# Kernel optimization log

Measured on AMD Instinct MI355X. Metric: run time of the kernel, lower is better.

The kernel has to match this reference:

```python
import jax, jax.numpy as jnp
import numpy as np

NUM_HIDDEN = 128
NUM_IN = 256
NUM_HEADS = 4
B, T, N, K = 4, 32, 96, 30


def setup_inputs() -> dict:
    key = jax.random.key(0)
    ks = jax.random.split(key, 7)
    return {
        "h_V": jax.random.normal(ks[0], (B, T, N, NUM_HIDDEN), dtype=jnp.float32),
        "h_EV": jax.random.normal(ks[1], (B, T, N, K, NUM_IN), dtype=jnp.float32),
        "mask_attend": jax.random.randint(ks[2], (B, T, N, K), 0, 2, dtype=jnp.int32),
        "Wq": jax.random.normal(ks[3], (NUM_HIDDEN, NUM_HIDDEN), dtype=jnp.float32) / np.sqrt(NUM_HIDDEN),
        "Wk": jax.random.normal(ks[4], (NUM_IN, NUM_HIDDEN), dtype=jnp.float32) / np.sqrt(NUM_IN),
        "Wv": jax.random.normal(ks[5], (NUM_IN, NUM_HIDDEN), dtype=jnp.float32) / np.sqrt(NUM_IN),
        "Wo": jax.random.normal(ks[6], (NUM_HIDDEN, NUM_HIDDEN), dtype=jnp.float32) / np.sqrt(NUM_HIDDEN),
    }


def reference(h_V, h_EV, mask_attend, Wq, Wk, Wv, Wo):
    b, t, n, k = h_EV.shape[:4]
    h = NUM_HEADS
    d = NUM_HIDDEN // h
    # projections
    Q = (h_V @ Wq).reshape(b, t, n, h, d)            # [B,T,N,H,d]
    Kp = (h_EV @ Wk).reshape(b, t, n, k, h, d)       # [B,T,N,K,H,d]
    V = (h_EV @ Wv).reshape(b, t, n, k, h, d)        # [B,T,N,K,H,d]
    # per-node neighbor attention logits [B,T,N,H,K]
    logits = jnp.einsum('btnhd,btnkhd->btnhk', Q, Kp) / jnp.sqrt(jnp.float32(d))
    neg_inf = jnp.finfo(jnp.float32).min
    mask = mask_attend[:, :, :, None, :]             # [B,T,N,1,K] -> broadcast over heads
    logits = jnp.where(mask > 0, logits, neg_inf)
    attend = jax.nn.softmax(logits, axis=-1)
    attend = attend * mask.astype(jnp.float32)
    # combine values: [B,T,N,H,d]
    out = jnp.einsum('btnhk,btnkhd->btnhd', attend, V).reshape(b, t, n, NUM_HIDDEN)
    return out @ Wo
```

## Files before the change

### kernel.cpp

```cpp
#include <hip/hip_runtime.h>
#include <hip/hip_bf16.h>
#include <cfloat>
#include <math.h>

constexpr int SITES = 12288;
constexpr int KNB   = 30;
constexpr int CIN   = 256;
#define RSQRT_D 0.17677669529663689f

typedef short bf16x8 __attribute__((ext_vector_type(8)));
typedef float f32x4  __attribute__((ext_vector_type(4)));

__device__ inline unsigned short f2bs(float x) {
    __hip_bfloat16 b = __float2bfloat16(x);
    return *(unsigned short*)&b;
}
__device__ inline float bs2f(unsigned short u) {
    unsigned int v = (unsigned int)u << 16;
    float f;
    __builtin_memcpy(&f, &v, 4);
    return f;
}
__device__ inline unsigned int pack2(float a, float b) {
    return (unsigned int)f2bs(a) | ((unsigned int)f2bs(b) << 16);
}

__global__ __launch_bounds__(256) void precompute_w(
    const float* __restrict__ Wq, const float* __restrict__ Wk,
    const float* __restrict__ Wv, const float* __restrict__ Wo,
    unsigned short* __restrict__ Mt, unsigned short* __restrict__ W3t) {
    int gid = blockIdx.x * 256 + threadIdx.x;
    if (gid < 131072) {
        int p = gid >> 7;
        int i = gid & 127;
        int h = p >> 8;
        int c = p & 255;
        const float4* wq = (const float4*)(Wq + (size_t)i * 128 + h * 32);
        const float4* wk = (const float4*)(Wk + (size_t)c * 128 + h * 32);
        float s = 0.f;
        #pragma unroll
        for (int d = 0; d < 8; ++d) {
            float4 a = wq[d], b = wk[d];
            s += a.x * b.x; s += a.y * b.y; s += a.z * b.z; s += a.w * b.w;
        }
        Mt[gid] = f2bs(s);
    } else {
        int o = gid - 131072;
        int p = o >> 7;
        int j = o & 127;
        int h = p >> 8;
        int c = p & 255;
        const float* wv = Wv + (size_t)c * 128 + h * 32;
        const float* wo = Wo + (size_t)(h * 32) * 128 + j;
        float s = 0.f;
        #pragma unroll
        for (int d = 0; d < 32; ++d)
            s += wv[d] * wo[(size_t)d * 128];
        W3t[(size_t)j * 1024 + p] = f2bs(s);
    }
}

template <bool OUT_BF16, bool A_F32>
__global__ __launch_bounds__(256) void gemm_bt_bf16(
    const void* __restrict__ Aptr, const unsigned short* __restrict__ Bt,
    void* __restrict__ C, int M, int N, int K) {
    constexpr int BM = 64, BN = 128, BK = 32, PAD = 8;
    constexpr int NT = BN / 16;
    __shared__ unsigned short As[BM][BK + PAD];
    __shared__ unsigned short Bs[BN][BK + PAD];
    const int tid  = threadIdx.x;
    const int wave = tid >> 6;
    const int lane = tid & 63;
    const int quad = lane >> 4;
    const int l16  = lane & 15;
    const int bm0 = blockIdx.x * BM;
    const int bn0 = blockIdx.y * BN;

    f32x4 acc[NT];
    #pragma unroll
    for (int j = 0; j < NT; ++j) acc[j] = (f32x4){0.f, 0.f, 0.f, 0.f};

    for (int kk = 0; kk < K; kk += BK) {
        {
            int row = tid >> 2, off = (tid & 3) * 8;
            if (A_F32) {
                const float* Af = (const float*)Aptr;
                const float4* src = (const float4*)&Af[(size_t)(bm0 + row) * K + kk + off];
                float4 a0 = src[0], a1 = src[1];
                uint4 p;
                p.x = pack2(a0.x, a0.y); p.y = pack2(a0.z, a0.w);
                p.z = pack2(a1.x, a1.y); p.w = pack2(a1.z, a1.w);
                *(uint4*)&As[row][off] = p;
            } else {
                const unsigned short* Ab = (const unsigned short*)Aptr;
                *(uint4*)&As[row][off] =
                    *(const uint4*)&Ab[(size_t)(bm0 + row) * K + kk + off];
            }
        }
        #pragma unroll
        for (int i = 0; i < 2; ++i) {
            int c2 = tid * 2 + i;
            int brow = c2 >> 2, boff = (c2 & 3) * 8;
            *(uint4*)&Bs[brow][boff] =
                *(const uint4*)&Bt[(size_t)(bn0 + brow) * K + kk + boff];
        }
        __syncthreads();
        bf16x8 af = *(const bf16x8*)&As[wave * 16 + l16][quad * 8];
        #pragma unroll
        for (int j = 0; j < NT; ++j) {
            bf16x8 bf = *(const bf16x8*)&Bs[j * 16 + l16][quad * 8];
            acc[j] = __builtin_amdgcn_mfma_f32_16x16x32_bf16(af, bf, acc[j], 0, 0, 0);
        }
        __syncthreads();
    }
    int row0 = bm0 + wave * 16 + quad * 4;
    #pragma unroll
    for (int j = 0; j < NT; ++j) {
        int col = bn0 + j * 16 + l16;
        #pragma unroll
        for (int r = 0; r < 4; ++r) {
            if (OUT_BF16)
                ((unsigned short*)C)[(size_t)(row0 + r) * N + col] = f2bs(acc[j][r]);
            else
                ((float*)C)[(size_t)(row0 + r) * N + col] = acc[j][r];
        }
    }
}

__global__ __launch_bounds__(256) void attn_kernel(
    const float* __restrict__ hEV, const int* __restrict__ mask,
    const unsigned short* __restrict__ qt, unsigned short* __restrict__ evb) {
    __shared__ unsigned short evS[KNB * CIN];
    __shared__ float qS[1024];
    __shared__ float logitsL[4 * 32];
    __shared__ float attendL[4 * 32];
    __shared__ int   activeS[32];
    __shared__ int   naS;

    const int s = blockIdx.x;
    const int tid = threadIdx.x;
    const int lane = tid & 63;
    const int wv = tid >> 6;
    const int hw = lane >> 5;
    const int sl = lane & 31;

    if (tid < 64) {
        int mk = (tid < KNB) ? mask[(size_t)s * KNB + tid] : 0;
        unsigned long long bal = __ballot(mk > 0);
        if (tid == 0) naS = __popcll(bal);
        if (mk > 0) activeS[__popcll(bal & ((1ull << tid) - 1))] = tid;
    } else if (tid < 192) {
        int t2 = tid - 64;
        uint4 u = ((const uint4*)(qt + (size_t)s * 1024))[t2];
        float f[8];
        f[0] = bs2f(u.x & 0xffff); f[1] = bs2f(u.x >> 16);
        f[2] = bs2f(u.y & 0xffff); f[3] = bs2f(u.y >> 16);
        f[4] = bs2f(u.z & 0xffff); f[5] = bs2f(u.z >> 16);
        f[6] = bs2f(u.w & 0xffff); f[7] = bs2f(u.w >> 16);
        *(float4*)&qS[t2 * 8]     = *(float4*)&f[0];
        *(float4*)&qS[t2 * 8 + 4] = *(float4*)&f[4];
    }
    __syncthreads();

    float qf[4][8];
    #pragma unroll
    for (int h = 0; h < 4; ++h) {
        *(float4*)&qf[h][0] = *(const float4*)&qS[h * 256 + sl * 8];
        *(float4*)&qf[h][4] = *(const float4*)&qS[h * 256 + sl * 8 + 4];
    }
    const int na = naS;

    for (int r = wv * 2 + hw; r < na; r += 8) {
        int k = activeS[r];
        const float* row = hEV + (size_t)s * (KNB * CIN) + (size_t)k * CIN + sl * 8;
        float4 v0 = *(const float4*)row;
        float4 v1 = *(const float4*)(row + 4);

        uint4 p;
        p.x = pack2(v0.x, v0.y); p.y = pack2(v0.z, v0.w);
        p.z = pack2(v1.x, v1.y); p.w = pack2(v1.z, v1.w);
        *(uint4*)&evS[r * CIN + sl * 8] = p;

        float l[4];
        #pragma unroll
        for (int h = 0; h < 4; ++h) {
            l[h] = v0.x * qf[h][0] + v0.y * qf[h][1] + v0.z * qf[h][2] + v0.w * qf[h][3]
                 + v1.x * qf[h][4] + v1.y * qf[h][5] + v1.z * qf[h][6] + v1.w * qf[h][7];
        }
        #pragma unroll
        for (int m = 1; m < 32; m <<= 1) {
            #pragma unroll
            for (int h = 0; h < 4; ++h) l[h] += __shfl_xor(l[h], m, 64);
        }
        if (sl == 0) {
            #pragma unroll
            for (int h = 0; h < 4; ++h) logitsL[h * 32 + r] = l[h] * RSQRT_D;
        }
    }
    __syncthreads();

    {
        float lg = (lane < na) ? logitsL[wv * 32 + lane] : -FLT_MAX;
        float mx = lg;
        #pragma unroll
        for (int m = 1; m < 64; m <<= 1) mx = fmaxf(mx, __shfl_xor(mx, m, 64));
        float e = (lane < na) ? __expf(lg - mx) : 0.f;
        float sm = e;
        #pragma unroll
        for (int m = 1; m < 64; m <<= 1) sm += __shfl_xor(sm, m, 64);
        if (lane < na) attendL[wv * 32 + lane] = e / sm;
    }
    __syncthreads();

    float a0 = 0.f, a1 = 0.f, a2 = 0.f, a3 = 0.f;
    for (int r = 0; r < na; ++r) {
        float evv = bs2f(evS[r * CIN + tid]);
        a0 = fmaf(attendL[r], evv, a0);
        a1 = fmaf(attendL[32 + r], evv, a1);
        a2 = fmaf(attendL[64 + r], evv, a2);
        a3 = fmaf(attendL[96 + r], evv, a3);
    }
    size_t ob = (size_t)s * 1024 + tid;
    evb[ob]       = f2bs(a0);
    evb[ob + 256] = f2bs(a1);
    evb[ob + 512] = f2bs(a2);
    evb[ob + 768] = f2bs(a3);
}

extern "C" void kernel_launch(void* const* d_in, const int* in_sizes, int n_in,
                              void* d_out, int out_size, void* d_ws, size_t ws_size,
                              hipStream_t stream) {
    const float* hV   = (const float*)d_in[0];
    const float* hEV  = (const float*)d_in[1];
    const int*   mask = (const int*)d_in[2];
    const float* Wq   = (const float*)d_in[3];
    const float* Wk   = (const float*)d_in[4];
    const float* Wv   = (const float*)d_in[5];
    const float* Wo   = (const float*)d_in[6];
    float* out = (float*)d_out;

    unsigned short* ws = (unsigned short*)d_ws;
    unsigned short* Mt   = ws;
    unsigned short* W3t  = ws + 131072;
    unsigned short* qt   = ws + 262144;
    unsigned short* evb  = qt + (size_t)SITES * 1024;
    size_t need = ((size_t)262144 + 2 * (size_t)SITES * 1024) * 2;
    if (ws_size < need) return;

    precompute_w<<<dim3(1024), dim3(256), 0, stream>>>(Wq, Wk, Wv, Wo, Mt, W3t);

    gemm_bt_bf16<true, true><<<dim3(SITES / 64, 1024 / 128), dim3(256), 0, stream>>>(
        hV, Mt, qt, SITES, 1024, 128);

    attn_kernel<<<dim3(SITES), dim3(256), 0, stream>>>(hEV, mask, qt, evb);

    gemm_bt_bf16<false, false><<<dim3(SITES / 64, 1), dim3(256), 0, stream>>>(
        evb, W3t, out, SITES, 128, 1024);
}
```

Baseline: 511.9 us.

## Prefetch GEMM tiles, split-K final GEMM with atomics, batch attention row loads

The GEMM kernel now prefetches the next K-slice of A and B into registers while the current tile is consumed. The final projection GEMM is split along K into four chunks that accumulate into the output with atomic adds. The output is zeroed by extra blocks added to the weight-precompute kernel. The Q GEMM uses a wider BN=256 tile, and the attention kernel issues all of a thread's neighbour-row loads up front before computing logits. The aim is more memory-level parallelism and better occupancy for the final GEMM, which had only 192 blocks. In exchange it adds atomic traffic, nondeterministic summation order, and more registers per thread.

Measured after the change: 531.9 us. +3.9%, slower.

```diff
diff --git a/kernel.cpp b/kernel.cpp
--- a/kernel.cpp
+++ b/kernel.cpp
@@ -28,7 +28,16 @@
 __global__ __launch_bounds__(256) void precompute_w(
     const float* __restrict__ Wq, const float* __restrict__ Wk,
     const float* __restrict__ Wv, const float* __restrict__ Wo,
-    unsigned short* __restrict__ Mt, unsigned short* __restrict__ W3t) {
+    unsigned short* __restrict__ Mt, unsigned short* __restrict__ W3t,
+    float* __restrict__ outZ) {
+    if (blockIdx.x >= 1024) {
+        int idx = (blockIdx.x - 1024) * 256 + threadIdx.x;
+        float4 z = {0.f, 0.f, 0.f, 0.f};
+        float4* o4 = (float4*)outZ;
+        #pragma unroll
+        for (int j = 0; j < 4; ++j) o4[(size_t)j * 98304 + idx] = z;
+        return;
+    }
     int gid = blockIdx.x * 256 + threadIdx.x;
     if (gid < 131072) {
         int p = gid >> 7;
@@ -60,12 +69,13 @@
     }
 }
 
-template <bool OUT_BF16, bool A_F32>
+template <int BN, bool OUT_BF16, bool A_F32, bool ATOMIC>
 __global__ __launch_bounds__(256) void gemm_bt_bf16(
     const void* __restrict__ Aptr, const unsigned short* __restrict__ Bt,
-    void* __restrict__ C, int M, int N, int K) {
-    constexpr int BM = 64, BN = 128, BK = 32, PAD = 8;
-    constexpr int NT = BN / 16;
+    void* __restrict__ C, int M, int N, int K, int Kc) {
+    constexpr int BM = 64, BK = 32, PAD = 8;
+    constexpr int NT  = BN / 16;
+    constexpr int BCH = (BN * BK) / (8 * 256);
     __shared__ unsigned short As[BM][BK + PAD];
     __shared__ unsigned short Bs[BN][BK + PAD];
     const int tid  = threadIdx.x;
@@ -75,41 +85,64 @@
     const int l16  = lane & 15;
     const int bm0 = blockIdx.x * BM;
     const int bn0 = blockIdx.y * BN;
+    const int k0  = blockIdx.z * Kc;
+    const int arow = tid >> 2, aoff = (tid & 3) * 8;
 
     f32x4 acc[NT];
     #pragma unroll
     for (int j = 0; j < NT; ++j) acc[j] = (f32x4){0.f, 0.f, 0.f, 0.f};
 
-    for (int kk = 0; kk < K; kk += BK) {
-        {
-            int row = tid >> 2, off = (tid & 3) * 8;
+    const float* Af = (const float*)Aptr;
+    const unsigned short* Ab = (const unsigned short*)Aptr;
+
+    float4 af0, af1; uint4 apre; uint4 bpre[BCH];
+    {
+        if (A_F32) {
+            const float4* src = (const float4*)&Af[(size_t)(bm0 + arow) * K + k0 + aoff];
+            af0 = src[0]; af1 = src[1];
+        } else {
+            apre = *(const uint4*)&Ab[(size_t)(bm0 + arow) * K + k0 + aoff];
+        }
+        #pragma unroll
+        for (int i = 0; i < BCH; ++i) {
+            int c2 = i * 256 + tid;
+            bpre[i] = *(const uint4*)&Bt[(size_t)(bn0 + (c2 >> 2)) * K + k0 + (c2 & 3) * 8];
+        }
+    }
+    for (int kk = k0; kk < k0 + Kc; kk += BK) {
+        if (A_F32) {
+            uint4 p;
+            p.x = pack2(af0.x, af0.y); p.y = pack2(af0.z, af0.w);
+            p.z = pack2(af1.x, af1.y); p.w = pack2(af1.z, af1.w);
+            *(uint4*)&As[arow][aoff] = p;
+        } else {
+            *(uint4*)&As[arow][aoff] = apre;
+        }
+        #pragma unroll
+        for (int i = 0; i < BCH; ++i) {
+            int c2 = i * 256 + tid;
+            *(uint4*)&Bs[c2 >> 2][(c2 & 3) * 8] = bpre[i];
+        }
+        __syncthreads();
+        int kn = kk + BK;
+        if (kn < k0 + Kc) {
             if (A_F32) {
-                const float* Af = (const float*)Aptr;
-                const float4* src = (const float4*)&Af[(size_t)(bm0 + row) * K + kk + off];
-                float4 a0 = src[0], a1 = src[1];
-                uint4 p;
-                p.x = pack2(a0.x, a0.y); p.y = pack2(a0.z, a0.w);
-                p.z = pack2(a1.x, a1.y); p.w = pack2(a1.z, a1.w);
-                *(uint4*)&As[row][off] = p;
+                const float4* src = (const float4*)&Af[(size_t)(bm0 + arow) * K + kn + aoff];
+                af0 = src[0]; af1 = src[1];
             } else {
-                const unsigned short* Ab = (const unsigned short*)Aptr;
-                *(uint4*)&As[row][off] =
-                    *(const uint4*)&Ab[(size_t)(bm0 + row) * K + kk + off];
-            }
-        }
-        #pragma unroll
-        for (int i = 0; i < 2; ++i) {
-            int c2 = tid * 2 + i;
-            int brow = c2 >> 2, boff = (c2 & 3) * 8;
-            *(uint4*)&Bs[brow][boff] =
-                *(const uint4*)&Bt[(size_t)(bn0 + brow) * K + kk + boff];
-        }
-        __syncthreads();
-        bf16x8 af = *(const bf16x8*)&As[wave * 16 + l16][quad * 8];
+                apre = *(const uint4*)&Ab[(size_t)(bm0 + arow) * K + kn + aoff];
+            }
+            #pragma unroll
+            for (int i = 0; i < BCH; ++i) {
+                int c2 = i * 256 + tid;
+                bpre[i] = *(const uint4*)&Bt[(size_t)(bn0 + (c2 >> 2)) * K + kn + (c2 & 3) * 8];
+            }
+        }
+        bf16x8 afr = *(const bf16x8*)&As[wave * 16 + l16][quad * 8];
         #pragma unroll
         for (int j = 0; j < NT; ++j) {
-            bf16x8 bf = *(const bf16x8*)&Bs[j * 16 + l16][quad * 8];
-            acc[j] = __builtin_amdgcn_mfma_f32_16x16x32_bf16(af, bf, acc[j], 0, 0, 0);
+            bf16x8 bfr = *(const bf16x8*)&Bs[j * 16 + l16][quad * 8];
+            acc[j] = __builtin_amdgcn_mfma_f32_16x16x32_bf16(afr, bfr, acc[j], 0, 0, 0);
         }
         __syncthreads();
     }
@@ -119,10 +152,13 @@
         int col = bn0 + j * 16 + l16;
         #pragma unroll
         for (int r = 0; r < 4; ++r) {
-            if (OUT_BF16)
-                ((unsigned short*)C)[(size_t)(row0 + r) * N + col] = f2bs(acc[j][r]);
+            size_t idx = (size_t)(row0 + r) * N + col;
+            if (ATOMIC)
+                unsafeAtomicAdd(&((float*)C)[idx], acc[j][r]);
+            else if (OUT_BF16)
+                ((unsigned short*)C)[idx] = f2bs(acc[j][r]);
             else
-                ((float*)C)[(size_t)(row0 + r) * N + col] = acc[j][r];
+                ((float*)C)[idx] = acc[j][r];
         }
     }
 }
@@ -170,31 +206,44 @@
     }
     const int na = naS;
 
-    for (int r = wv * 2 + hw; r < na; r += 8) {
-        int k = activeS[r];
-        const float* row = hEV + (size_t)s * (KNB * CIN) + (size_t)k * CIN + sl * 8;
-        float4 v0 = *(const float4*)row;
-        float4 v1 = *(const float4*)(row + 4);
-
-        uint4 p;
-        p.x = pack2(v0.x, v0.y); p.y = pack2(v0.z, v0.w);
-        p.z = pack2(v1.x, v1.y); p.w = pack2(v1.z, v1.w);
-        *(uint4*)&evS[r * CIN + sl * 8] = p;
-
-        float l[4];
-        #pragma unroll
-        for (int h = 0; h < 4; ++h) {
-            l[h] = v0.x * qf[h][0] + v0.y * qf[h][1] + v0.z * qf[h][2] + v0.w * qf[h][3]
-                 + v1.x * qf[h][4] + v1.y * qf[h][5] + v1.z * qf[h][6] + v1.w * qf[h][7];
-        }
-        #pragma unroll
-        for (int m = 1; m < 32; m <<= 1) {
+    const float* base = hEV + (size_t)s * (KNB * CIN) + sl * 8;
+    float4 va[4], vb[4];
+    int rw[4];
+    #pragma unroll
+    for (int i = 0; i < 4; ++i) {
+        int r = wv * 2 + hw + i * 8;
+        rw[i] = (r < na) ? r : -1;
+        if (r < na) {
+            const float* row = base + (size_t)activeS[r] * CIN;
+            va[i] = *(const float4*)row;
+            vb[i] = *(const float4*)(row + 4);
+        }
+    }
+    #pragma unroll
+    for (int i = 0; i < 4; ++i) {
+        if (rw[i] >= 0) {
+            int r = rw[i];
+            float4 v0 = va[i], v1 = vb[i];
+            uint4 p;
+            p.x = pack2(v0.x, v0.y); p.y = pack2(v0.z, v0.w);
+            p.z = pack2(v1.x, v1.y); p.w = pack2(v1.z, v1.w);
+            *(uint4*)&evS[r * CIN + sl * 8] = p;
+
+            float l[4];
             #pragma unroll
-            for (int h = 0; h < 4; ++h) l[h] += __shfl_xor(l[h], m, 64);
-        }
-        if (sl == 0) {
+            for (int h = 0; h < 4; ++h) {
+                l[h] = v0.x * qf[h][0] + v0.y * qf[h][1] + v0.z * qf[h][2] + v0.w * qf[h][3]
+                     + v1.x * qf[h][4] + v1.y * qf[h][5] + v1.z * qf[h][6] + v1.w * qf[h][7];
+            }
             #pragma unroll
-            for (int h = 0; h < 4; ++h) logitsL[h * 32 + r] = l[h] * RSQRT_D;
+            for (int m = 1; m < 32; m <<= 1) {
+                #pragma unroll
+                for (int h = 0; h < 4; ++h) l[h] += __shfl_xor(l[h], m, 64);
+            }
+            if (sl == 0) {
+                #pragma unroll
+                for (int h = 0; h < 4; ++h) logitsL[h * 32 + r] = l[h] * RSQRT_D;
+            }
         }
     }
     __syncthreads();
@@ -247,13 +296,15 @@
     size_t need = ((size_t)262144 + 2 * (size_t)SITES * 1024) * 2;
     if (ws_size < need) return;
 
-    precompute_w<<<dim3(1024), dim3(256), 0, stream>>>(Wq, Wk, Wv, Wo, Mt, W3t);
-
-    gemm_bt_bf16<true, true><<<dim3(SITES / 64, 1024 / 128), dim3(256), 0, stream>>>(
-        hV, Mt, qt, SITES, 1024, 128);
+    precompute_w<<<dim3(1408), dim3(256), 0, stream>>>(Wq, Wk, Wv, Wo, Mt, W3t, out);
+
+    gemm_bt_bf16<256, true, true, false>
+        <<<dim3(SITES / 64, 1024 / 256, 1), dim3(256), 0, stream>>>(
+            hV, Mt, qt, SITES, 1024, 128, 128);
 
     attn_kernel<<<dim3(SITES), dim3(256), 0, stream>>>(hEV, mask, qt, evb);
 
-    gemm_bt_bf16<false, false><<<dim3(SITES / 64, 1), dim3(256), 0, stream>>>(
-        evb, W3t, out, SITES, 128, 1024);
-}
+    gemm_bt_bf16<128, false, false, true>
+        <<<dim3(SITES / 64, 1, 4), dim3(256), 0, stream>>>(
+            evb, W3t, out, SITES, 128, 1024, 256);
+}
```
